# Performance work log

Measured on AMD Instinct MI355X. Metric: run time of the kernel, lower is better.

The kernel has to match this reference:

```python
import jax, jax.numpy as jnp
import numpy as np

B, S, D, C = 1024, 200, 64, 256  # batch, max_seq_length_all, reshape_size, codebook_size


def setup_inputs() -> dict:
    key = jax.random.key(0)
    k1, k2, k3 = jax.random.split(key, 3)
    rq_item_embeddings = jax.random.normal(k1, (B, S, D), dtype=jnp.float32)
    labels = jax.random.randint(k2, (B, S), 0, C, dtype=jnp.int32)
    attention_mask = jax.random.randint(k3, (B, S), 0, 2, dtype=jnp.int32)
    return {
        "rq_item_embeddings": rq_item_embeddings,
        "labels": labels,
        "attention_mask": attention_mask,
    }


def reference(rq_item_embeddings, labels, attention_mask):
    # Batched version of the original per-sample loop:
    #   M[c, s] = 1 if labels[s] == c, masked by attention_mask[s]
    #   M <- L1-normalize over seq dim (divide each cluster row by its count)
    #   cluster_emb = M @ sample  (per-cluster mean of item embeddings)
    x = rq_item_embeddings  # [B, S, D]
    mask = attention_mask.astype(x.dtype)  # [B, S]
    # one-hot cluster assignment, [B, C, S]
    one_hot = (labels[:, None, :] == jnp.arange(C, dtype=labels.dtype)[None, :, None])
    cluster_mask = one_hot.astype(x.dtype) * mask[:, None, :]  # [B, C, S]
    counts = cluster_mask.sum(axis=-1)  # [B, C]  (== L1 norm of each row)
    inv = jnp.where(counts > 0, 1.0 / jnp.maximum(counts, 1.0), 0.0)  # [B, C]
    # normalized scatter matrix @ embeddings -> per-cluster mean, [B, C, D]
    cluster_emb = jnp.einsum('bcs,bsd->bcd', cluster_mask, x) * inv[:, :, None]
    return cluster_emb, cluster_mask.astype(jnp.int32)
```

## Files before the change

kernel.cpp:

```cpp
#include <hip/hip_runtime.h>

#define NB 1024
#define NS 200
#define ND 64
#define NC 256

typedef float v4f __attribute__((ext_vector_type(4)));

__global__ __launch_bounds__(256) void s3rec_cluster_kernel(
    const float* __restrict__ x,
    const int*   __restrict__ labels,
    const int*   __restrict__ amask,
    float* __restrict__ out_emb,
    float* __restrict__ out_mask)
{
    __shared__ __align__(16) float s_emb[NC * ND];
    __shared__ int   s_lab[NS];
    __shared__ float s_inv[NC];

    const int b = blockIdx.x;
    const int t = threadIdx.x;

    for (int i = t; i < NS; i += 256) {
        const int l = labels[b * NS + i];
        const int m = amask [b * NS + i];
        s_lab[i] = (m != 0) ? l : -1;
    }
    for (int i = t; i < NC * ND; i += 256) s_emb[i] = 0.0f;
    __syncthreads();

    v4f* om4 = reinterpret_cast<v4f*>(out_mask + (size_t)b * (NC * NS));
    for (int i4 = t; i4 < (NC * NS) / 4; i4 += 256) {
        const int c  = i4 / 50;
        const int s0 = (i4 - c * 50) * 4;
        v4f v;
        v.x = (s_lab[s0 + 0] == c) ? 1.0f : 0.0f;
        v.y = (s_lab[s0 + 1] == c) ? 1.0f : 0.0f;
        v.z = (s_lab[s0 + 2] == c) ? 1.0f : 0.0f;
        v.w = (s_lab[s0 + 3] == c) ? 1.0f : 0.0f;
        __builtin_nontemporal_store(v, &om4[i4]);
    }

    const int lane = t & 63;
    const int w    = t >> 6;
    const float* xb = x + (size_t)b * NS * ND;
    for (int s = w; s < NS; s += 4) {
        const int c = s_lab[s];
        if (c >= 0) {
            atomicAdd(&s_emb[c * ND + lane], xb[s * ND + lane]);
        }
    }

    int cnt = 0;
    for (int s = 0; s < NS; ++s) cnt += (s_lab[s] == t) ? 1 : 0;
    s_inv[t] = (cnt > 0) ? (1.0f / (float)cnt) : 0.0f;
    __syncthreads();

    v4f* oe4 = reinterpret_cast<v4f*>(out_emb + (size_t)b * (NC * ND));
    const v4f* se4 = reinterpret_cast<const v4f*>(s_emb);
    for (int i4 = t; i4 < (NC * ND) / 4; i4 += 256) {
        const float inv = s_inv[i4 >> 4];
        v4f v = se4[i4];
        v *= inv;
        __builtin_nontemporal_store(v, &oe4[i4]);
    }
}

extern "C" void kernel_launch(void* const* d_in, const int* in_sizes, int n_in,
                              void* d_out, int out_size, void* d_ws, size_t ws_size,
                              hipStream_t stream) {
    const float* x      = (const float*)d_in[0];
    const int*   labels = (const int*)  d_in[1];
    const int*   amask  = (const int*)  d_in[2];

    float* out_emb  = (float*)d_out;
    float* out_mask = out_emb + (size_t)NB * NC * ND;

    s3rec_cluster_kernel<<<dim3(NB), dim3(256), 0, stream>>>(
        x, labels, amask, out_emb, out_mask);
}
```

Baseline: 353.0 us.

## Split work into mask-writer and gather-sum blocks, drop 64KB LDS accumulator

```diff
diff --git a/kernel.cpp b/kernel.cpp
--- a/kernel.cpp
+++ b/kernel.cpp
@@ -7,62 +7,98 @@
 
 typedef float v4f __attribute__((ext_vector_type(4)));
 
-__global__ __launch_bounds__(256) void s3rec_cluster_kernel(
+__global__ __launch_bounds__(256, 8) void s3rec_cluster_kernel(
     const float* __restrict__ x,
     const int*   __restrict__ labels,
     const int*   __restrict__ amask,
     float* __restrict__ out_emb,
     float* __restrict__ out_mask)
 {
-    __shared__ __align__(16) float s_emb[NC * ND];
-    __shared__ int   s_lab[NS];
+    __shared__ __align__(16) int s_lab[NS];
+    __shared__ int   s_cnt[NC];
+    __shared__ int   s_off[NC];
     __shared__ float s_inv[NC];
+    __shared__ int   s_list[NS];
+    __shared__ int   s_part[4];
 
-    const int b = blockIdx.x;
-    const int t = threadIdx.x;
+    const int role = blockIdx.x % 3;
+    const int b    = blockIdx.x / 3;
+    const int t    = threadIdx.x;
 
     for (int i = t; i < NS; i += 256) {
         const int l = labels[b * NS + i];
         const int m = amask [b * NS + i];
         s_lab[i] = (m != 0) ? l : -1;
     }
-    for (int i = t; i < NC * ND; i += 256) s_emb[i] = 0.0f;
+
+    if (role < 2) {
+        __syncthreads();
+        v4f* om4 = reinterpret_cast<v4f*>(out_mask + (size_t)b * (NC * NS));
+        const int i4lo = role * 6400;
+        #pragma unroll 5
+        for (int k = 0; k < 25; ++k) {
+            const int i4 = i4lo + k * 256 + t;
+            const int c  = i4 / 50;
+            const int s0 = (i4 - c * 50) * 4;
+            const int4 lv = *reinterpret_cast<const int4*>(&s_lab[s0]);
+            v4f v;
+            v.x = (lv.x == c) ? 1.0f : 0.0f;
+            v.y = (lv.y == c) ? 1.0f : 0.0f;
+            v.z = (lv.z == c) ? 1.0f : 0.0f;
+            v.w = (lv.w == c) ? 1.0f : 0.0f;
+            __builtin_nontemporal_store(v, &om4[i4]);
+        }
+        return;
+    }
+
+    s_cnt[t] = 0;
     __syncthreads();
-
-    v4f* om4 = reinterpret_cast<v4f*>(out_mask + (size_t)b * (NC * NS));
-    for (int i4 = t; i4 < (NC * NS) / 4; i4 += 256) {
-        const int c  = i4 / 50;
-        const int s0 = (i4 - c * 50) * 4;
-        v4f v;
-        v.x = (s_lab[s0 + 0] == c) ? 1.0f : 0.0f;
-        v.y = (s_lab[s0 + 1] == c) ? 1.0f : 0.0f;
-        v.z = (s_lab[s0 + 2] == c) ? 1.0f : 0.0f;
-        v.w = (s_lab[s0 + 3] == c) ? 1.0f : 0.0f;
-        __builtin_nontemporal_store(v, &om4[i4]);
+    if (t < NS) {
+        const int l = s_lab[t];
+        if (l >= 0) atomicAdd(&s_cnt[l], 1);
     }
+    __syncthreads();
 
     const int lane = t & 63;
     const int w    = t >> 6;
-    const float* xb = x + (size_t)b * NS * ND;
-    for (int s = w; s < NS; s += 4) {
-        const int c = s_lab[s];
-        if (c >= 0) {
-            atomicAdd(&s_emb[c * ND + lane], xb[s * ND + lane]);
+    const int cnt  = s_cnt[t];
+    s_inv[t] = (cnt > 0) ? (1.0f / (float)cnt) : 0.0f;
+
+    int v = cnt;
+    #pragma unroll
+    for (int d = 1; d < 64; d <<= 1) {
+        const int n = __shfl_up(v, d, 64);
+        if (lane >= d) v += n;
+    }
+    if (lane == 63) s_part[w] = v;
+    __syncthreads();
+    int base = 0;
+    for (int i = 0; i < w; ++i) base += s_part[i];
+    s_off[t] = base + v - cnt;
+    __syncthreads();
+
+    if (t < NS) {
+        const int L = s_lab[t];
+        if (L >= 0) {
+            int r = 0;
+            for (int s2 = 0; s2 < t; ++s2) r += (s_lab[s2] == L) ? 1 : 0;
+            s_list[s_off[L] + r] = t;
         }
     }
-
-    int cnt = 0;
-    for (int s = 0; s < NS; ++s) cnt += (s_lab[s] == t) ? 1 : 0;
-    s_inv[t] = (cnt > 0) ? (1.0f / (float)cnt) : 0.0f;
     __syncthreads();
 
-    v4f* oe4 = reinterpret_cast<v4f*>(out_emb + (size_t)b * (NC * ND));
-    const v4f* se4 = reinterpret_cast<const v4f*>(s_emb);
-    for (int i4 = t; i4 < (NC * ND) / 4; i4 += 256) {
-        const float inv = s_inv[i4 >> 4];
-        v4f v = se4[i4];
-        v *= inv;
-        __builtin_nontemporal_store(v, &oe4[i4]);
+    const float* xb = x + (size_t)b * NS * ND;
+    float* oe = out_emb + (size_t)b * (NC * ND);
+    const int cend = w * 64 + 64;
+    for (int c = w * 64; c < cend; ++c) {
+        const int n = s_cnt[c];
+        const int o = s_off[c];
+        float acc = 0.0f;
+        for (int j = 0; j < n; ++j) {
+            const int s = s_list[o + j];
+            acc += xb[s * ND + lane];
+        }
+        __builtin_nontemporal_store(acc * s_inv[c], &oe[c * ND + lane]);
     }
 }
 
@@ -76,6 +112,6 @@
     float* out_emb  = (float*)d_out;
     float* out_mask = out_emb + (size_t)NB * NC * ND;
 
-    s3rec_cluster_kernel<<<dim3(NB), dim3(256), 0, stream>>>(
+    s3rec_cluster_kernel<<<dim3(NB * 3), dim3(256), 0, stream>>>(
         x, labels, amask, out_emb, out_mask);
 }
```

Result: faster. 330.0 us (-6.5%).
